# Kernel tuning notes

Measured on AMD Instinct MI355X. Metric: run time of the kernel, lower is better.

## Reference

```python
import jax, jax.numpy as jnp
import numpy as np

B, S, D = 2, 1024, 1024
L, E, F = 2, 8, 2048


def setup_inputs() -> dict:
    key = jax.random.key(0)
    kx, kp, k1, k2 = jax.random.split(key, 4)
    x = jax.random.normal(kx, (B, S, D), dtype=jnp.float32)
    # prototypes scaled so dot products are O(1), keeping softmax well-behaved
    protos = jax.random.normal(kp, (L, E, D), dtype=jnp.float32) / np.sqrt(D)
    W1 = jax.random.normal(k1, (L, E, D, F), dtype=jnp.float32) * 0.02
    W2 = jax.random.normal(k2, (L, E, F, D), dtype=jnp.float32) * 0.02
    return {"x": x, "protos": protos, "W1": W1, "W2": W2, "k": 2}


def _route(x, protos_l, k):
    # expert_mapping: abs(dot(prototype, input)) per expert, keep top-k, rest -> -inf, softmax
    scores = jnp.abs(jnp.einsum("bsd,ed->bse", x, protos_l))  # [B,S,E]
    topv, _ = jax.lax.top_k(scores, k)
    thresh = topv[..., -1:]  # k-th largest per token
    masked = jnp.where(scores >= thresh, scores, -jnp.inf)
    return jax.nn.softmax(masked, axis=-1)  # [B,S,E]


def reference(x, protos, W1, W2, k):
    n_layers = protos.shape[0]
    for l in range(n_layers):  # fixed small layer loop
        w = _route(x, protos[l], k)  # [B,S,E]
        h = jax.nn.relu(jnp.einsum("bsd,edf->bsef", x, W1[l]))  # [B,S,E,F]
        y = jnp.einsum("bsef,efd,bse->bsd", h, W2[l], w)  # weighted expert mix
        x = x + y
    return x
```

## Files before the change

kernel.cpp:

```cpp
#include <hip/hip_runtime.h>
#include <hip/hip_bf16.h>
#include <cstdint>

#define T_TOKENS 2048
#define DDIM 1024
#define FDIM 2048
#define NEXP 8
#define NLAYER 2
#define BMPAD 64
#define RMAX 4608
#define RALLOC 4736

#define ATILE_EL 2048
#define BTILE_EL 4096

typedef unsigned short u16;
typedef short bf16x8 __attribute__((ext_vector_type(8)));
typedef u16 u16x8 __attribute__((ext_vector_type(8)));
typedef u16 u16x4v __attribute__((ext_vector_type(4)));
typedef float f32x4 __attribute__((ext_vector_type(4)));

__device__ __forceinline__ u16 bf16_rn(float f) {
  unsigned u = __builtin_bit_cast(unsigned, f);
  u += 0x7fffu + ((u >> 16) & 1u);
  return (u16)(u >> 16);
}
__device__ __forceinline__ float bf16_f(u16 h) {
  unsigned u = ((unsigned)h) << 16;
  return __builtin_bit_cast(float, u);
}

__device__ __forceinline__ void gl16(const void* g, void* l) {
  __builtin_amdgcn_global_load_lds((const __attribute__((address_space(1))) void*)g,
                                   (__attribute__((address_space(3))) void*)l, 16, 0, 0);
}

__device__ __forceinline__ void xcd_swizzle(int& bx, int& by, int& bz) {
  const unsigned gx = gridDim.x, gy = gridDim.y;
  const unsigned lin = blockIdx.x + gx * (blockIdx.y + gy * blockIdx.z);
  const unsigned nwg = gx * gy * gridDim.z;
  const unsigned nl = (lin & 7u) * (nwg >> 3) + (lin >> 3);
  bx = nl % gx;
  const unsigned t = nl / gx;
  by = t % gy;
  bz = t / gy;
}

__global__ __launch_bounds__(256) void route_kernel(
    const float* __restrict__ x, const float* __restrict__ protos,
    int* __restrict__ eid, float* __restrict__ wgt) {
  const int t = blockIdx.x;
  const int tid = threadIdx.x;
  const float4* xr4 = (const float4*)(x + (size_t)t * DDIM);
  const float4* pr4 = (const float4*)protos;
  __shared__ float red[NEXP][256];
  const float4 xv = xr4[tid];
  float acc[NEXP];
#pragma unroll
  for (int e = 0; e < NEXP; ++e) {
    const float4 p = pr4[e * 256 + tid];
    acc[e] = xv.x * p.x + xv.y * p.y + xv.z * p.z + xv.w * p.w;
  }
#pragma unroll
  for (int e = 0; e < NEXP; ++e) red[e][tid] = acc[e];
  __syncthreads();
  for (int s = 128; s > 0; s >>= 1) {
    if (tid < s) {
#pragma unroll
      for (int e = 0; e < NEXP; ++e) red[e][tid] += red[e][tid + s];
    }
    __syncthreads();
  }
  if (tid == 0) {
    float m1 = -1.f, m2 = -1.f;
    int i1 = 0, i2 = 0;
#pragma unroll
    for (int e = 0; e < NEXP; ++e) {
      float s = fabsf(red[e][0]);
      if (s > m1) { m2 = m1; i2 = i1; m1 = s; i1 = e; }
      else if (s > m2) { m2 = s; i2 = e; }
    }
    float e2 = __expf(m2 - m1);
    float z = 1.f + e2;
    eid[t * 2] = i1;
    eid[t * 2 + 1] = i2;
    wgt[t * 2] = 1.f / z;
    wgt[t * 2 + 1] = e2 / z;
  }
}

__global__ __launch_bounds__(256) void compact_kernel(
    const int* __restrict__ eid, int* __restrict__ cnt, int* __restrict__ offp,
    int* __restrict__ row2token, int* __restrict__ pos) {
  __shared__ int lcnt[NEXP][256];
  __shared__ int s_off[NEXP], s_tot[NEXP];
  const int tid = threadIdx.x;
  const int base = tid * 16;

  int my[16];
#pragma unroll
  for (int i = 0; i < 4; ++i)
    *(int4*)&my[i * 4] = *(const int4*)(eid + base + i * 4);

#pragma unroll
  for (int e = 0; e < NEXP; ++e) {
    int c = 0;
#pragma unroll
    for (int i = 0; i < 16; ++i) c += (my[i] == e) ? 1 : 0;
    lcnt[e][tid] = c;
  }

  for (int r = tid; r < RMAX; r += 256) row2token[r] = -1;
  __syncthreads();

  if (tid < NEXP) {
    int run = 0;
    for (int i = 0; i < 256; ++i) {
      int v = lcnt[tid][i];
      lcnt[tid][i] = run;
      run += v;
    }
    s_tot[tid] = run;
  }
  __syncthreads();
  if (tid == 0) {
    int o = 0;
    for (int e = 0; e < NEXP; ++e) {
      s_off[e] = o;
      o += (s_tot[e] + BMPAD - 1) & ~(BMPAD - 1);
    }
  }
  __syncthreads();

  int myoff[NEXP];
#pragma unroll
  for (int e = 0; e < NEXP; ++e) myoff[e] = s_off[e] + lcnt[e][tid];
#pragma unroll
  for (int i = 0; i < 16; ++i) {
    int r = 0;
#pragma unroll
    for (int e = 0; e < NEXP; ++e) r = (my[i] == e) ? myoff[e] : r;
    row2token[r] = (base + i) >> 1;
    pos[base + i] = r;
#pragma unroll
    for (int e = 0; e < NEXP; ++e) myoff[e] += (my[i] == e) ? 1 : 0;
  }

  if (tid < NEXP) {
    cnt[tid] = s_tot[tid];
    offp[tid] = s_off[tid];
  }
}

__global__ __launch_bounds__(256) void gather_kernel(
    const float* __restrict__ x, const int* __restrict__ row2token,
    u16* __restrict__ Ahi, u16* __restrict__ Alo) {
  const int r = blockIdx.x;
  const int t = row2token[r];
  const int c = threadIdx.x * 4;
  float4 v = make_float4(0.f, 0.f, 0.f, 0.f);
  if (t >= 0) v = *(const float4*)(x + (size_t)t * DDIM + c);
  float vv[4] = {v.x, v.y, v.z, v.w};
  u16x4v hi, lo;
#pragma unroll
  for (int i = 0; i < 4; ++i) {
    u16 h = bf16_rn(vv[i]);
    hi[i] = h;
    lo[i] = bf16_rn(vv[i] - bf16_f(h));
  }
  const size_t el = ((size_t)(r >> 6) * (DDIM >> 5) + (c >> 5)) * ATILE_EL +
                    (size_t)(((c >> 3) & 3) * 64 + (r & 63)) * 8 + (c & 7);
  *(u16x4v*)(Ahi + el) = hi;
  *(u16x4v*)(Alo + el) = lo;
}

template <bool LO>
__global__ __launch_bounds__(256) void wconv_kernel(
    const float* __restrict__ W, u16* __restrict__ Hi, u16* __restrict__ Lo,
    int K, int N) {
  const int e = blockIdx.z, nb = blockIdx.x, kb = blockIdx.y;
  const float* Wp = W + ((size_t)e * K + (size_t)kb * 32) * N + nb * 128;
  __shared__ float tile[32][129];
  const int t = threadIdx.x;
#pragma unroll
  for (int i = 0; i < 4; ++i) {
    const int f4 = i * 256 + t;
    const int kr = f4 >> 5;
    const int c4 = (f4 & 31) * 4;
    float4 v = *(const float4*)(Wp + (size_t)kr * N + c4);
    *(float4*)&tile[kr][c4] = v;
  }
  __syncthreads();
  const size_t tb = (((size_t)e * (N >> 7) + nb) * (K >> 5) + kb) * BTILE_EL;
#pragma unroll
  for (int j = 0; j < 2; ++j) {
    const int cid = j * 256 + t;
    const int n = cid & 127, ksel = cid >> 7;
    u16x8 hv, lv;
#pragma unroll
    for (int i = 0; i < 8; ++i) {
      float f = tile[ksel * 8 + i][n];
      u16 h = bf16_rn(f);
      hv[i] = h;
      if (LO) lv[i] = bf16_rn(f - bf16_f(h));
    }
    *(u16x8*)(Hi + tb + (size_t)cid * 8) = hv;
    if (LO) *(u16x8*)(Lo + tb + (size_t)cid * 8) = lv;
  }
}

template <bool RELU, int OUTMODE>
__global__ __launch_bounds__(256, 3) void gemm_split(
    const u16* __restrict__ Ahi, const u16* __restrict__ Alo,
    const u16* __restrict__ Bhi, const u16* __restrict__ Blo,
    u16* __restrict__ OutHi, u16* __restrict__ OutLo, float* __restrict__ OutF,
    const int* __restrict__ cnt, const int* __restrict__ offp, int K, int N) {
  int bx, by, bz;
  xcd_swizzle(bx, by, bz);
  const int e = bz;
  const int cp = (cnt[e] + 63) & ~63;
  if (by * 64 >= cp) return;
  const int row0 = offp[e] + by * 64;
  const int n0 = bx * 128;
  const int nkb = K >> 5;

  constexpr int BUF_EL = 12288;
  __shared__ u16 lds[2 * BUF_EL];

  const int tid = threadIdx.x;
  const int lane = tid & 63;
  const int wid = tid >> 6;
  const int wr = wid >> 1, wc = wid & 1;
  const int lr = lane & 15, kg = lane >> 4;
  const int lo16 = lane << 4;

  f32x4 acc[2][4];
#pragma unroll
  for (int i = 0; i < 2; ++i)
#pragma unroll
    for (int j = 0; j < 4; ++j)
#pragma unroll
      for (int r = 0; r < 4; ++r) acc[i][j][r] = 0.f;

  const size_t abase = (size_t)(row0 >> 6) * nkb;
  const size_t bbase = ((size_t)e * (N >> 7) + (n0 >> 7)) * nkb;

  auto STAGE = [&](int kb, int b) {
    char* d = (char*)(lds + b * BUF_EL);
    if (wid == 0) {
      const char* gh = (const char*)(Ahi + (abase + kb) * ATILE_EL);
      const char* gl = (const char*)(Alo + (abase + kb) * ATILE_EL);
#pragma unroll
      for (int i = 0; i < 4; ++i) gl16(gh + i * 1024 + lo16, d + i * 1024);
#pragma unroll
      for (int i = 0; i < 4; ++i) gl16(gl + i * 1024 + lo16, d + 4096 + i * 1024);
    } else if (wid == 1) {
      const char* g = (const char*)(Bhi + (bbase + kb) * BTILE_EL);
#pragma unroll
      for (int i = 0; i < 8; ++i) gl16(g + i * 1024 + lo16, d + 8192 + i * 1024);
    } else if (wid == 2) {
      const char* g = (const char*)(Blo + (bbase + kb) * BTILE_EL);
#pragma unroll
      for (int i = 0; i < 8; ++i) gl16(g + i * 1024 + lo16, d + 16384 + i * 1024);
    }
  };

  STAGE(0, 0);
  __syncthreads();

  int cur = 0;
  for (int kb = 0; kb < nkb; ++kb) {
    if (kb + 1 < nkb) STAGE(kb + 1, cur ^ 1);

    const u16* buf = lds + cur * BUF_EL;
    const u16* AsH = buf;
    const u16* AsL = buf + 2048;
    const u16* BsH = buf + 4096;
    const u16* BsL = buf + 8192;
    const int arow = (kg * 64 + wr * 32 + lr) * 8;
    const int bcol = (kg * 128 + wc * 64 + lr) * 8;

    bf16x8 ah0 = *(const bf16x8*)&AsH[arow];
    bf16x8 ah1 = *(const bf16x8*)&AsH[arow + 128];
    bf16x8 bh[4];
#pragma unroll
    for (int j = 0; j < 4; ++j) bh[j] = *(const bf16x8*)&BsH[bcol + j * 128];
#pragma unroll
    for (int j = 0; j < 4; ++j) {
      acc[0][j] = __builtin_amdgcn_mfma_f32_16x16x32_bf16(ah0, bh[j], acc[0][j], 0, 0, 0);
      acc[1][j] = __builtin_amdgcn_mfma_f32_16x16x32_bf16(ah1, bh[j], acc[1][j], 0, 0, 0);
    }
    bf16x8 al0 = *(const bf16x8*)&AsL[arow];
    bf16x8 al1 = *(const bf16x8*)&AsL[arow + 128];
#pragma unroll
    for (int j = 0; j < 4; ++j) {
      bf16x8 bl = *(const bf16x8*)&BsL[bcol + j * 128];
      acc[0][j] = __builtin_amdgcn_mfma_f32_16x16x32_bf16(ah0, bl, acc[0][j], 0, 0, 0);
      acc[1][j] = __builtin_amdgcn_mfma_f32_16x16x32_bf16(ah1, bl, acc[1][j], 0, 0, 0);
      acc[0][j] = __builtin_amdgcn_mfma_f32_16x16x32_bf16(al0, bh[j], acc[0][j], 0, 0, 0);
      acc[1][j] = __builtin_amdgcn_mfma_f32_16x16x32_bf16(al1, bh[j], acc[1][j], 0, 0, 0);
    }
    __syncthreads();
    cur ^= 1;
  }

  const int nkbO = N >> 5;
#pragma unroll
  for (int i = 0; i < 2; ++i) {
#pragma unroll
    for (int j = 0; j < 4; ++j) {
      const int Cj = n0 + wc * 64 + j * 16 + lr;
      f32x4 v = acc[i][j];
#pragma unroll
      for (int r = 0; r < 4; ++r) {
        const int R = row0 + wr * 32 + i * 16 + kg * 4 + r;
        float f = v[r];
        if (RELU) f = fmaxf(f, 0.f);
        if constexpr (OUTMODE == 0) {
          OutF[(size_t)R * N + Cj] = f;
        } else {
          const size_t el = ((size_t)(R >> 6) * nkbO + (Cj >> 5)) * ATILE_EL +
                            (size_t)(((Cj >> 3) & 3) * 64 + (R & 63)) * 8 + (Cj & 7);
          u16 h = bf16_rn(f);
          OutHi[el] = h;
          OutLo[el] = bf16_rn(f - bf16_f(h));
        }
      }
    }
  }
}

template <bool RELU, int OUTMODE, int SKF>
__global__ __launch_bounds__(256, 4) void gemm_plain(
    const u16* __restrict__ Ahi, const u16* __restrict__ Bhi,
    u16* __restrict__ OutHi, float* __restrict__ OutF,
    const int* __restrict__ cnt, const int* __restrict__ offp, int K, int N) {
  int bx, by, bz;
  xcd_swizzle(bx, by, bz);
  const int e = bz / SKF, sk = bz % SKF;
  const int cp = (cnt[e] + 63) & ~63;
  if (by * 128 >= cp) return;
  const int row0 = offp[e] + by * 128;
  const int rend = offp[e] + cp;
  const int n0 = bx * 128;
  const int nkb = K >> 5;
  const int kbN = nkb / SKF;
  const int kb0 = sk * kbN;

  constexpr int BUF_EL = 8192;
  __shared__ u16 lds[2 * BUF_EL];

  const int tid = threadIdx.x;
  const int lane = tid & 63;
  const int wid = tid >> 6;
  const int wr = wid >> 1, wc = wid & 1;
  const int lr = lane & 15, kg = lane >> 4;
  const int lo16 = lane << 4;

  f32x4 acc[4][4];
#pragma unroll
  for (int i = 0; i < 4; ++i)
#pragma unroll
    for (int j = 0; j < 4; ++j)
#pragma unroll
      for (int r = 0; r < 4; ++r) acc[i][j][r] = 0.f;

  const int at0 = row0 >> 6;
  const size_t bbase = ((size_t)e * (N >> 7) + (n0 >> 7)) * nkb;

  auto STAGE = [&](int kb, int b) {
    char* d = (char*)(lds + b * BUF_EL);
    if (wid < 2) {
      const char* g = (const char*)(Ahi + ((size_t)(at0 + wid) * nkb + kb) * ATILE_EL);
#pragma unroll
      for (int i = 0; i < 4; ++i) gl16(g + i * 1024 + lo16, d + wid * 4096 + i * 1024);
    } else {
      const char* g = (const char*)(Bhi + (bbase + kb) * BTILE_EL) + (wid - 2) * 4096;
#pragma unroll
      for (int i = 0; i < 4; ++i) gl16(g + i * 1024 + lo16, d + 8192 + (wid - 2) * 4096 + i * 1024);
    }
  };

  STAGE(kb0, 0);
  __syncthreads();

  int cur = 0;
  for (int kb = kb0; kb < kb0 + kbN; ++kb) {
    if (kb + 1 < kb0 + kbN) STAGE(kb + 1, cur ^ 1);

    const u16* buf = lds + cur * BUF_EL;
    const u16* AsH = buf + wr * 2048;
    const u16* BsH = buf + 4096;
    const int arow = (kg * 64 + lr) * 8;
    const int bcol = (kg * 128 + wc * 64 + lr) * 8;

    bf16x8 ah[4], bh[4];
#pragma unroll
    for (int i = 0; i < 4; ++i) ah[i] = *(const bf16x8*)&AsH[arow + i * 128];
#pragma unroll
    for (int j = 0; j < 4; ++j) bh[j] = *(const bf16x8*)&BsH[bcol + j * 128];
#pragma unroll
    for (int i = 0; i < 4; ++i)
#pragma unroll
      for (int j = 0; j < 4; ++j)
        acc[i][j] = __builtin_amdgcn_mfma_f32_16x16x32_bf16(ah[i], bh[j], acc[i][j], 0, 0, 0);
    __syncthreads();
    cur ^= 1;
  }

  const int nkbO = N >> 5;
#pragma unroll
  for (int i = 0; i < 4; ++i) {
#pragma unroll
    for (int j = 0; j < 4; ++j) {
      const int Cj = n0 + wc * 64 + j * 16 + lr;
      f32x4 v = acc[i][j];
#pragma unroll
      for (int r = 0; r < 4; ++r) {
        const int R = row0 + wr * 64 + i * 16 + kg * 4 + r;
        if (R >= rend) continue;
        float f = v[r];
        if (RELU) f = fmaxf(f, 0.f);
        if constexpr (OUTMODE == 0) {
          OutF[((size_t)sk * RALLOC + R) * N + Cj] = f;
        } else {
          const size_t el = ((size_t)(R >> 6) * nkbO + (Cj >> 5)) * ATILE_EL +
                            (size_t)(((Cj >> 3) & 3) * 64 + (R & 63)) * 8 + (Cj & 7);
          OutHi[el] = bf16_rn(f);
        }
      }
    }
  }
}

template <int NPART>
__global__ __launch_bounds__(256) void apply_kernel(
    const float* __restrict__ part, const int* __restrict__ pos,
    const float* __restrict__ wgt, float* __restrict__ x) {
  const int t = blockIdx.x;
  const int c = threadIdx.x * 4;
  const int p0 = pos[t * 2], p1 = pos[t * 2 + 1];
  const float w0 = wgt[t * 2], w1 = wgt[t * 2 + 1];
  float4 xa = *(float4*)(x + (size_t)t * DDIM + c);
  float4 y0 = *(const float4*)(part + (size_t)p0 * DDIM + c);
  float4 y1 = *(const float4*)(part + (size_t)p1 * DDIM + c);
  if (NPART == 2) {
    const float* P1 = part + (size_t)RALLOC * DDIM;
    const float4 b0 = *(const float4*)(P1 + (size_t)p0 * DDIM + c);
    const float4 b1 = *(const float4*)(P1 + (size_t)p1 * DDIM + c);
    y0.x += b0.x; y0.y += b0.y; y0.z += b0.z; y0.w += b0.w;
    y1.x += b1.x; y1.y += b1.y; y1.z += b1.z; y1.w += b1.w;
  }
  xa.x += w0 * y0.x + w1 * y1.x;
  xa.y += w0 * y0.y + w1 * y1.y;
  xa.z += w0 * y0.z + w1 * y1.z;
  xa.w += w0 * y0.w + w1 * y1.w;
  *(float4*)(x + (size_t)t * DDIM + c) = xa;
}

extern "C" void kernel_launch(void* const* d_in, const int* in_sizes, int n_in,
                              void* d_out, int out_size, void* d_ws, size_t ws_size,
                              hipStream_t stream) {
  const float* x = (const float*)d_in[0];
  const float* protos = (const float*)d_in[1];
  const float* W1 = (const float*)d_in[2];
  const float* W2 = (const float*)d_in[3];
  float* xcur = (float*)d_out;

  u16* W_hi = (u16*)d_ws;
  u16* W_lo = W_hi + (size_t)NEXP * DDIM * FDIM;
  u16* Ag_hi = W_lo + (size_t)NEXP * DDIM * FDIM;
  u16* Ag_lo = Ag_hi + (size_t)RALLOC * DDIM;
  u16* h_hi = Ag_lo + (size_t)RALLOC * DDIM;
  u16* h_lo = h_hi + (size_t)RALLOC * FDIM;
  float* part = (float*)(h_lo + (size_t)RALLOC * FDIM);
  float* wgt = part + (size_t)2 * RALLOC * DDIM;
  int* eid = (int*)(wgt + T_TOKENS * 2);
  int* pos = eid + T_TOKENS * 2;
  int* cnt = pos + T_TOKENS * 2;
  int* offp = cnt + NEXP;
  int* row2token = offp + NEXP;

  hipMemcpyAsync(xcur, x, (size_t)T_TOKENS * DDIM * sizeof(float),
                 hipMemcpyDeviceToDevice, stream);

  for (int l = 0; l < NLAYER; ++l) {
    route_kernel<<<T_TOKENS, 256, 0, stream>>>(
        xcur, protos + (size_t)l * NEXP * DDIM, eid, wgt);
    compact_kernel<<<1, 256, 0, stream>>>(eid, cnt, offp, row2token, pos);
    gather_kernel<<<RMAX, 256, 0, stream>>>(xcur, row2token, Ag_hi, Ag_lo);
    const float* W1l = W1 + (size_t)l * NEXP * DDIM * FDIM;
    const float* W2l = W2 + (size_t)l * NEXP * FDIM * DDIM;
    if (l == 0) {
      wconv_kernel<true><<<dim3(FDIM / 128, DDIM / 32, NEXP), 256, 0, stream>>>(
          W1l, W_hi, W_lo, DDIM, FDIM);
      gemm_split<true, 1><<<dim3(FDIM / 128, RMAX / 64, NEXP), 256, 0, stream>>>(
          Ag_hi, Ag_lo, W_hi, W_lo, h_hi, h_lo, nullptr, cnt, offp, DDIM, FDIM);
      wconv_kernel<true><<<dim3(DDIM / 128, FDIM / 32, NEXP), 256, 0, stream>>>(
          W2l, W_hi, W_lo, FDIM, DDIM);
      gemm_split<false, 0><<<dim3(DDIM / 128, RMAX / 64, NEXP), 256, 0, stream>>>(
          h_hi, h_lo, W_hi, W_lo, nullptr, nullptr, part, cnt, offp, FDIM, DDIM);
      apply_kernel<1><<<T_TOKENS, 256, 0, stream>>>(part, pos, wgt, xcur);
    } else {
      wconv_kernel<false><<<dim3(FDIM / 128, DDIM / 32, NEXP), 256, 0, stream>>>(
          W1l, W_hi, nullptr, DDIM, FDIM);
      gemm_plain<true, 2, 1><<<dim3(FDIM / 128, RMAX / 128, NEXP), 256, 0, stream>>>(
          Ag_hi, W_hi, h_hi, nullptr, cnt, offp, DDIM, FDIM);
      wconv_kernel<false><<<dim3(DDIM / 128, FDIM / 32, NEXP), 256, 0, stream>>>(
          W2l, W_hi, nullptr, FDIM, DDIM);
      gemm_plain<false, 0, 2><<<dim3(DDIM / 128, RMAX / 128, NEXP * 2), 256, 0, stream>>>(
          h_hi, W_hi, nullptr, part, cnt, offp, FDIM, DDIM);
      apply_kernel<2><<<T_TOKENS, 256, 0, stream>>>(part, pos, wgt, xcur);
    }
  }
}
```

Baseline: 371.8 us.

## Precompute layer-1 routing algebraically so layer-0 down-projection can use plain bf16

The layer-0 down-projection GEMM switches from the split hi/lo bf16 GEMM (three MFMAs per step) to the single-pass bf16 GEMM with split-K. To keep layer-1 routing accurate despite that lower precision, layer-1 scores are computed as protos2·x0 plus a weighted sum of the split-precision h times P, where P = W2·protos2ᵀ for every expert pair. P is computed inside a new weight-conversion kernel and then reduced. The layer-1 gather also stops producing the unused low half. This adds extra kernels and partial-sum traffic for P, and the residual update in layer 0 now carries bf16 error.

```diff
diff --git a/kernel.cpp b/kernel.cpp
--- a/kernel.cpp
+++ b/kernel.cpp
@@ -89,6 +89,78 @@
   }
 }
 
+__global__ __launch_bounds__(256) void route2_kernel(
+    const float* __restrict__ x, const float* __restrict__ protos2,
+    const u16* __restrict__ h_hi, const u16* __restrict__ h_lo,
+    const float* __restrict__ P, const int* __restrict__ eidA,
+    const int* __restrict__ pos, const float* __restrict__ wgtA,
+    int* __restrict__ eidB, float* __restrict__ wgtB) {
+  const int t = blockIdx.x;
+  const int tid = threadIdx.x;
+  __shared__ float red[NEXP][256];
+  const float4 xv = ((const float4*)(x + (size_t)t * DDIM))[tid];
+  float acc[NEXP];
+#pragma unroll
+  for (int e = 0; e < NEXP; ++e) {
+    const float4 p = ((const float4*)protos2)[e * 256 + tid];
+    acc[e] = xv.x * p.x + xv.y * p.y + xv.z * p.z + xv.w * p.w;
+  }
+  const int p0 = pos[t * 2], p1 = pos[t * 2 + 1];
+  const int e0 = eidA[t * 2], e1 = eidA[t * 2 + 1];
+  const float w0 = wgtA[t * 2], w1 = wgtA[t * 2 + 1];
+  const int f0 = tid * 8;
+  const int nkbF = FDIM >> 5;
+  float h0[8], h1[8];
+  {
+    const size_t el0 = ((size_t)(p0 >> 6) * nkbF + (f0 >> 5)) * ATILE_EL +
+                       (size_t)((((f0 >> 3) & 3) * 64 + (p0 & 63)) * 8);
+    const size_t el1 = ((size_t)(p1 >> 6) * nkbF + (f0 >> 5)) * ATILE_EL +
+                       (size_t)((((f0 >> 3) & 3) * 64 + (p1 & 63)) * 8);
+    u16x8 a = *(const u16x8*)&h_hi[el0], b = *(const u16x8*)&h_lo[el0];
+    u16x8 c = *(const u16x8*)&h_hi[el1], d = *(const u16x8*)&h_lo[el1];
+#pragma unroll
+    for (int j = 0; j < 8; ++j) {
+      h0[j] = bf16_f(a[j]) + bf16_f(b[j]);
+      h1[j] = bf16_f(c[j]) + bf16_f(d[j]);
+    }
+  }
+#pragma unroll
+  for (int e2 = 0; e2 < NEXP; ++e2) {
+    const float* P0 = P + ((size_t)(e0 * NEXP + e2)) * FDIM + f0;
+    const float* P1 = P + ((size_t)(e1 * NEXP + e2)) * FDIM + f0;
+    float c = 0.f;
+#pragma unroll
+    for (int j = 0; j < 8; ++j) c += w0 * h0[j] * P0[j] + w1 * h1[j] * P1[j];
+    acc[e2] += c;
+  }
+#pragma unroll
+  for (int e = 0; e < NEXP; ++e) red[e][tid] = acc[e];
+  __syncthreads();
+  for (int s = 128; s > 0; s >>= 1) {
+    if (tid < s) {
+#pragma unroll
+      for (int e = 0; e < NEXP; ++e) red[e][tid] += red[e][tid + s];
+    }
+    __syncthreads();
+  }
+  if (tid == 0) {
+    float m1 = -1.f, m2 = -1.f;
+    int i1 = 0, i2 = 0;
+#pragma unroll
+    for (int e = 0; e < NEXP; ++e) {
+      float s = fabsf(red[e][0]);
+      if (s > m1) { m2 = m1; i2 = i1; m1 = s; i1 = e; }
+      else if (s > m2) { m2 = s; i2 = e; }
+    }
+    float e2 = __expf(m2 - m1);
+    float z = 1.f + e2;
+    eidB[t * 2] = i1;
+    eidB[t * 2 + 1] = i2;
+    wgtB[t * 2] = 1.f / z;
+    wgtB[t * 2 + 1] = e2 / z;
+  }
+}
+
 __global__ __launch_bounds__(256) void compact_kernel(
     const int* __restrict__ eid, int* __restrict__ cnt, int* __restrict__ offp,
     int* __restrict__ row2token, int* __restrict__ pos) {
@@ -152,6 +224,7 @@
   }
 }
 
+template <bool LO>
 __global__ __launch_bounds__(256) void gather_kernel(
     const float* __restrict__ x, const int* __restrict__ row2token,
     u16* __restrict__ Ahi, u16* __restrict__ Alo) {
@@ -166,12 +239,12 @@
   for (int i = 0; i < 4; ++i) {
     u16 h = bf16_rn(vv[i]);
     hi[i] = h;
-    lo[i] = bf16_rn(vv[i] - bf16_f(h));
+    if (LO) lo[i] = bf16_rn(vv[i] - bf16_f(h));
   }
   const size_t el = ((size_t)(r >> 6) * (DDIM >> 5) + (c >> 5)) * ATILE_EL +
                     (size_t)(((c >> 3) & 3) * 64 + (r & 63)) * 8 + (c & 7);
   *(u16x4v*)(Ahi + el) = hi;
-  *(u16x4v*)(Alo + el) = lo;
+  if (LO) *(u16x4v*)(Alo + el) = lo;
 }
 
 template <bool LO>
@@ -209,11 +282,58 @@
   }
 }
 
-template <bool RELU, int OUTMODE>
+__global__ __launch_bounds__(256) void wconv_p_kernel(
+    const float* __restrict__ W, u16* __restrict__ Hi,
+    const float* __restrict__ proto2, float* __restrict__ Ppart, int K, int N) {
+  const int e = blockIdx.z, nb = blockIdx.x, kb = blockIdx.y;
+  const float* Wp = W + ((size_t)e * K + (size_t)kb * 32) * N + nb * 128;
+  __shared__ float tile[32][129];
+  __shared__ float pr[NEXP][128];
+  const int t = threadIdx.x;
+#pragma unroll
+  for (int i = 0; i < 4; ++i) {
+    const int f4 = i * 256 + t;
+    const int kr = f4 >> 5;
+    const int c4 = (f4 & 31) * 4;
+    float4 v = *(const float4*)(Wp + (size_t)kr * N + c4);
+    *(float4*)&tile[kr][c4] = v;
+  }
+  {
+    const int idx = t * 4;
+    const int e2 = idx >> 7, n = idx & 127;
+    *(float4*)&pr[e2][n] = *(const float4*)(proto2 + (size_t)e2 * DDIM + nb * 128 + n);
+  }
+  __syncthreads();
+  const size_t tb = (((size_t)e * (N >> 7) + nb) * (K >> 5) + kb) * BTILE_EL;
+#pragma unroll
+  for (int j = 0; j < 2; ++j) {
+    const int cid = j * 256 + t;
+    const int n = cid & 127, ksel = cid >> 7;
+    u16x8 hv;
+#pragma unroll
+    for (int i = 0; i < 8; ++i) hv[i] = bf16_rn(tile[ksel * 8 + i][n]);
+    *(u16x8*)(Hi + tb + (size_t)cid * 8) = hv;
+  }
+  const int e2 = t >> 5, f = t & 31;
+  float s = 0.f;
+#pragma unroll 16
+  for (int n = 0; n < 128; ++n) s += tile[f][n] * pr[e2][n];
+  Ppart[(((size_t)nb * NEXP + e) * NEXP + e2) * FDIM + kb * 32 + f] = s;
+}
+
+__global__ __launch_bounds__(256) void reduce_p_kernel(
+    const float* __restrict__ Ppart, float* __restrict__ P) {
+  const int i = blockIdx.x * 256 + threadIdx.x;
+  float s = 0.f;
+#pragma unroll
+  for (int nb = 0; nb < 8; ++nb) s += Ppart[(size_t)nb * (NEXP * NEXP * FDIM) + i];
+  P[i] = s;
+}
+
 __global__ __launch_bounds__(256, 3) void gemm_split(
     const u16* __restrict__ Ahi, const u16* __restrict__ Alo,
     const u16* __restrict__ Bhi, const u16* __restrict__ Blo,
-    u16* __restrict__ OutHi, u16* __restrict__ OutLo, float* __restrict__ OutF,
+    u16* __restrict__ OutHi, u16* __restrict__ OutLo,
     const int* __restrict__ cnt, const int* __restrict__ offp, int K, int N) {
   int bx, by, bz;
   xcd_swizzle(bx, by, bz);
@@ -314,17 +434,12 @@
 #pragma unroll
       for (int r = 0; r < 4; ++r) {
         const int R = row0 + wr * 32 + i * 16 + kg * 4 + r;
-        float f = v[r];
-        if (RELU) f = fmaxf(f, 0.f);
-        if constexpr (OUTMODE == 0) {
-          OutF[(size_t)R * N + Cj] = f;
-        } else {
-          const size_t el = ((size_t)(R >> 6) * nkbO + (Cj >> 5)) * ATILE_EL +
-                            (size_t)(((Cj >> 3) & 3) * 64 + (R & 63)) * 8 + (Cj & 7);
-          u16 h = bf16_rn(f);
-          OutHi[el] = h;
-          OutLo[el] = bf16_rn(f - bf16_f(h));
-        }
+        float f = fmaxf(v[r], 0.f);
+        const size_t el = ((size_t)(R >> 6) * nkbO + (Cj >> 5)) * ATILE_EL +
+                          (size_t)(((Cj >> 3) & 3) * 64 + (R & 63)) * 8 + (Cj & 7);
+        u16 h = bf16_rn(f);
+        OutHi[el] = h;
+        OutLo[el] = bf16_rn(f - bf16_f(h));
       }
     }
   }
@@ -433,7 +548,6 @@
   }
 }
 
-template <int NPART>
 __global__ __launch_bounds__(256) void apply_kernel(
     const float* __restrict__ part, const int* __restrict__ pos,
     const float* __restrict__ wgt, float* __restrict__ x) {
@@ -441,16 +555,14 @@
   const int c = threadIdx.x * 4;
   const int p0 = pos[t * 2], p1 = pos[t * 2 + 1];
   const float w0 = wgt[t * 2], w1 = wgt[t * 2 + 1];
+  const float* P1p = part + (size_t)RALLOC * DDIM;
   float4 xa = *(float4*)(x + (size_t)t * DDIM + c);
   float4 y0 = *(const float4*)(part + (size_t)p0 * DDIM + c);
   float4 y1 = *(const float4*)(part + (size_t)p1 * DDIM + c);
-  if (NPART == 2) {
-    const float* P1 = part + (size_t)RALLOC * DDIM;
-    const float4 b0 = *(const float4*)(P1 + (size_t)p0 * DDIM + c);
-    const float4 b1 = *(const float4*)(P1 + (size_t)p1 * DDIM + c);
-    y0.x += b0.x; y0.y += b0.y; y0.z += b0.z; y0.w += b0.w;
-    y1.x += b1.x; y1.y += b1.y; y1.z += b1.z; y1.w += b1.w;
-  }
+  const float4 b0 = *(const float4*)(P1p + (size_t)p0 * DDIM + c);
+  const float4 b1 = *(const float4*)(P1p + (size_t)p1 * DDIM + c);
+  y0.x += b0.x; y0.y += b0.y; y0.z += b0.z; y0.w += b0.w;
+  y1.x += b1.x; y1.y += b1.y; y1.z += b1.z; y1.w += b1.w;
   xa.x += w0 * y0.x + w1 * y1.x;
   xa.y += w0 * y0.y + w1 * y1.y;
   xa.z += w0 * y0.z + w1 * y1.z;
@@ -474,43 +586,48 @@
   u16* h_hi = Ag_lo + (size_t)RALLOC * DDIM;
   u16* h_lo = h_hi + (size_t)RALLOC * FDIM;
   float* part = (float*)(h_lo + (size_t)RALLOC * FDIM);
-  float* wgt = part + (size_t)2 * RALLOC * DDIM;
-  int* eid = (int*)(wgt + T_TOKENS * 2);
-  int* pos = eid + T_TOKENS * 2;
-  int* cnt = pos + T_TOKENS * 2;
+  float* Ppart = part + (size_t)2 * RALLOC * DDIM;
+  float* P = Ppart + (size_t)8 * NEXP * NEXP * FDIM;
+  float* wgtA = P + (size_t)NEXP * NEXP * FDIM;
+  float* wgtB = wgtA + T_TOKENS * 2;
+  int* eidA = (int*)(wgtB + T_TOKENS * 2);
+  int* eidB = eidA + T_TOKENS * 2;
+  int* posA = eidB + T_TOKENS * 2;
+  int* posB = posA + T_TOKENS * 2;
+  int* cnt = posB + T_TOKENS * 2;
   int* offp = cnt + NEXP;
   int* row2token = offp + NEXP;
 
   hipMemcpyAsync(xcur, x, (size_t)T_TOKENS * DDIM * sizeof(float),
                  hipMemcpyDeviceToDevice, stream);
 
-  for (int l = 0; l < NLAYER; ++l) {
-    route_kernel<<<T_TOKENS, 256, 0, stream>>>(
-        xcur, protos + (size_t)l * NEXP * DDIM, eid, wgt);
-    compact_kernel<<<1, 256, 0, stream>>>(eid, cnt, offp, row2token, pos);
-    gather_kernel<<<RMAX, 256, 0, stream>>>(xcur, row2token, Ag_hi, Ag_lo);
-    const float* W1l = W1 + (size_t)l * NEXP * DDIM * FDIM;
-    const float* W2l = W2 + (size_t)l * NEXP * FDIM * DDIM;
-    if (l == 0) {
-      wconv_kernel<true><<<dim3(FDIM / 128, DDIM / 32, NEXP), 256, 0, stream>>>(
-          W1l, W_hi, W_lo, DDIM, FDIM);
-      gemm_split<true, 1><<<dim3(FDIM / 128, RMAX / 64, NEXP), 256, 0, stream>>>(
-          Ag_hi, Ag_lo, W_hi, W_lo, h_hi, h_lo, nullptr, cnt, offp, DDIM, FDIM);
-      wconv_kernel<true><<<dim3(DDIM / 128, FDIM / 32, NEXP), 256, 0, stream>>>(
-          W2l, W_hi, W_lo, FDIM, DDIM);
-      gemm_split<false, 0><<<dim3(DDIM / 128, RMAX / 64, NEXP), 256, 0, stream>>>(
-          h_hi, h_lo, W_hi, W_lo, nullptr, nullptr, part, cnt, offp, FDIM, DDIM);
-      apply_kernel<1><<<T_TOKENS, 256, 0, stream>>>(part, pos, wgt, xcur);
-    } else {
-      wconv_kernel<false><<<dim3(FDIM / 128, DDIM / 32, NEXP), 256, 0, stream>>>(
-          W1l, W_hi, nullptr, DDIM, FDIM);
-      gemm_plain<true, 2, 1><<<dim3(FDIM / 128, RMAX / 128, NEXP), 256, 0, stream>>>(
-          Ag_hi, W_hi, h_hi, nullptr, cnt, offp, DDIM, FDIM);
-      wconv_kernel<false><<<dim3(DDIM / 128, FDIM / 32, NEXP), 256, 0, stream>>>(
-          W2l, W_hi, nullptr, FDIM, DDIM);
-      gemm_plain<false, 0, 2><<<dim3(DDIM / 128, RMAX / 128, NEXP * 2), 256, 0, stream>>>(
-          h_hi, W_hi, nullptr, part, cnt, offp, FDIM, DDIM);
-      apply_kernel<2><<<T_TOKENS, 256, 0, stream>>>(part, pos, wgt, xcur);
-    }
-  }
-}
+  const float* protos2 = protos + (size_t)NEXP * DDIM;
+
+  route_kernel<<<T_TOKENS, 256, 0, stream>>>(xcur, protos, eidA, wgtA);
+  compact_kernel<<<1, 256, 0, stream>>>(eidA, cnt, offp, row2token, posA);
+  gather_kernel<true><<<RMAX, 256, 0, stream>>>(xcur, row2token, Ag_hi, Ag_lo);
+  wconv_kernel<true><<<dim3(FDIM / 128, DDIM / 32, NEXP), 256, 0, stream>>>(
+      W1, W_hi, W_lo, DDIM, FDIM);
+  gemm_split<<<dim3(FDIM / 128, RMAX / 64, NEXP), 256, 0, stream>>>(
+      Ag_hi, Ag_lo, W_hi, W_lo, h_hi, h_lo, cnt, offp, DDIM, FDIM);
+  wconv_p_kernel<<<dim3(DDIM / 128, FDIM / 32, NEXP), 256, 0, stream>>>(
+      W2, W_hi, protos2, Ppart, FDIM, DDIM);
+  reduce_p_kernel<<<NEXP * NEXP * FDIM / 256, 256, 0, stream>>>(Ppart, P);
+  gemm_plain<false, 0, 2><<<dim3(DDIM / 128, RMAX / 128, NEXP * 2), 256, 0, stream>>>(
+      h_hi, W_hi, nullptr, part, cnt, offp, FDIM, DDIM);
+  route2_kernel<<<T_TOKENS, 256, 0, stream>>>(
+      xcur, protos2, h_hi, h_lo, P, eidA, posA, wgtA, eidB, wgtB);
+  apply_kernel<<<T_TOKENS, 256, 0, stream>>>(part, posA, wgtA, xcur);
+
+  compact_kernel<<<1, 256, 0, stream>>>(eidB, cnt, offp, row2token, posB);
+  gather_kernel<false><<<RMAX, 256, 0, stream>>>(xcur, row2token, Ag_hi, nullptr);
+  wconv_kernel<false><<<dim3(FDIM / 128, DDIM / 32, NEXP), 256, 0, stream>>>(
+      W1 + (size_t)NEXP * DDIM * FDIM, W_hi, nullptr, DDIM, FDIM);
+  gemm_plain<true, 2, 1><<<dim3(FDIM / 128, RMAX / 128, NEXP), 256, 0, stream>>>(
+      Ag_hi, W_hi, h_hi, nullptr, cnt, offp, DDIM, FDIM);
+  wconv_kernel<false><<<dim3(DDIM / 128, FDIM / 32, NEXP), 256, 0, stream>>>(
+      W2 + (size_t)NEXP * FDIM * DDIM, W_hi, nullptr, FDIM, DDIM);
+  gemm_plain<false, 0, 2><<<dim3(DDIM / 128, RMAX / 128, NEXP * 2), 256, 0, stream>>>(
+      h_hi, W_hi, nullptr, part, cnt, offp, FDIM, DDIM);
+  apply_kernel<<<T_TOKENS, 256, 0, stream>>>(part, posB, wgtB, xcur);
+}
```

After: 366.7 us. No clear change (-1.4%).
